# Performance work log

Measured on AMD Instinct MI355X. Metric: run time of the kernel, lower is better.

## Reference

```python
import jax, jax.numpy as jnp
import numpy as np

B, N, M = 256, 4096, 64
EPS = 1e-16

def setup_inputs() -> dict:
    key = jax.random.key(0)
    ks = jax.random.split(key, 9)
    memory = jax.random.normal(ks[0], (B, N, M), dtype=jnp.float32) * 0.1
    k = jax.random.normal(ks[1], (B, M), dtype=jnp.float32)
    beta = jax.random.uniform(ks[2], (B, 1), dtype=jnp.float32) * 5.0  # key strength > 0
    g = jax.random.uniform(ks[3], (B, 1), dtype=jnp.float32)           # gate in [0,1)
    s = jax.nn.softmax(jax.random.normal(ks[4], (B, 3), dtype=jnp.float32), axis=1)  # shift dist
    gamma = 1.0 + jax.random.uniform(ks[5], (B, 1), dtype=jnp.float32) * 2.0  # sharpen >= 1
    w_prev = jax.nn.softmax(jax.random.normal(ks[6], (B, N), dtype=jnp.float32), axis=1)
    e = jax.random.uniform(ks[7], (B, M), dtype=jnp.float32)  # erase in [0,1)
    a = jax.random.normal(ks[8], (B, M), dtype=jnp.float32)   # add vector
    return {"memory": memory, "k": k, "beta": beta, "g": g, "s": s,
            "gamma": gamma, "w_prev": w_prev, "e": e, "a": a}


def reference(memory, k, beta, g, s, gamma, w_prev, e, a):
    # --- address (section 3.3) ---
    # cosine similarity (torch F.cosine_similarity semantics: norms clamped at 1e-8)
    mem_e = memory + EPS                       # [B,N,M]
    k_e = (k + EPS)[:, None, :]                # [B,1,M]
    num = jnp.sum(mem_e * k_e, axis=-1)        # [B,N]
    mem_n = jnp.maximum(jnp.sqrt(jnp.sum(mem_e * mem_e, axis=-1)), 1e-8)
    k_n = jnp.maximum(jnp.sqrt(jnp.sum(k_e * k_e, axis=-1)), 1e-8)
    cos = num / (mem_n * k_n)                  # [B,N]
    wc = jax.nn.softmax(beta * cos, axis=1)    # content weighting
    # interpolate with previous weighting
    wg = g * wc + (1.0 - g) * w_prev           # [B,N]
    # circular convolution with 3-tap shift kernel s:
    # out[n] = s0*wg[n-1] + s1*wg[n] + s2*wg[n+1]  (circular)
    w_hat = (s[:, 0:1] * jnp.roll(wg, 1, axis=1)
             + s[:, 1:2] * wg
             + s[:, 2:3] * jnp.roll(wg, -1, axis=1))
    # sharpen
    wp = w_hat ** gamma
    w = wp / (jnp.sum(wp, axis=1, keepdims=True) + EPS)
    # --- read (section 3.1) ---
    rd = jnp.einsum('bn,bnm->bm', w, memory)
    # --- write (section 3.2): erase then add via outer products ---
    erase = w[:, :, None] * e[:, None, :]      # [B,N,M]
    add = w[:, :, None] * a[:, None, :]        # [B,N,M]
    new_mem = memory * (1.0 - erase) + add
    return rd, new_mem, w
```

## Files before the change

### kernel.cpp

```cpp
#include <hip/hip_runtime.h>
#include <math.h>

#define Bdim 256
#define Ndim 4096
#define Mdim 64
#define EPSF 1e-16f

__global__ __launch_bounds__(256) void pass_a_kernel(
    const float* __restrict__ mem, const float* __restrict__ k,
    float* __restrict__ q)
{
    const int blocks_per_b = Ndim / 64;
    const int b = blockIdx.x / blocks_per_b;
    const int rowbase = (blockIdx.x % blocks_per_b) * 64;
    const int t = threadIdx.x;
    const int m4 = t & 15;
    const int rsub = t >> 4;

    float4 ke = reinterpret_cast<const float4*>(k + b * Mdim)[m4];
    ke.x += EPSF; ke.y += EPSF; ke.z += EPSF; ke.w += EPSF;

    const float4* memb = reinterpret_cast<const float4*>(mem + (size_t)b * Ndim * Mdim);

    #pragma unroll
    for (int it = 0; it < 4; ++it) {
        const int row = rowbase + it * 16 + rsub;
        float4 mv = memb[row * 16 + m4];
        mv.x += EPSF; mv.y += EPSF; mv.z += EPSF; mv.w += EPSF;
        float d  = mv.x * ke.x + mv.y * ke.y + mv.z * ke.z + mv.w * ke.w;
        float nr = mv.x * mv.x + mv.y * mv.y + mv.z * mv.z + mv.w * mv.w;
        #pragma unroll
        for (int mask = 1; mask < 16; mask <<= 1) {
            d  += __shfl_xor(d, mask);
            nr += __shfl_xor(nr, mask);
        }
        if (m4 == 0) {
            const float mn = fmaxf(sqrtf(nr), 1e-8f);
            q[b * Ndim + row] = d / mn;
        }
    }
}

__device__ __forceinline__ float block_reduce_sum(float v, float* red, int t)
{
    const int lane = t & 63, wave = t >> 6;
    #pragma unroll
    for (int mask = 32; mask; mask >>= 1) v += __shfl_xor(v, mask);
    __syncthreads();
    if (lane == 0) red[wave] = v;
    __syncthreads();
    return red[0] + red[1] + red[2] + red[3];
}

__device__ __forceinline__ float block_reduce_max(float v, float* red, int t)
{
    const int lane = t & 63, wave = t >> 6;
    #pragma unroll
    for (int mask = 32; mask; mask >>= 1) v = fmaxf(v, __shfl_xor(v, mask));
    __syncthreads();
    if (lane == 0) red[wave] = v;
    __syncthreads();
    return fmaxf(fmaxf(red[0], red[1]), fmaxf(red[2], red[3]));
}

__global__ __launch_bounds__(256) void pass_b_kernel(
    const float* __restrict__ q, const float* __restrict__ k,
    const float* __restrict__ beta, const float* __restrict__ g,
    const float* __restrict__ s, const float* __restrict__ gamma,
    const float* __restrict__ w_prev, float* __restrict__ w_out)
{
    __shared__ float wg_lds[Ndim];
    __shared__ float red[4];
    __shared__ float sh_kn;

    const int b = blockIdx.x;
    const int t = threadIdx.x;
    const int lane = t & 63, wave = t >> 6;

    if (wave == 0) {
        float v = k[b * Mdim + lane] + EPSF;
        float sq = v * v;
        #pragma unroll
        for (int mask = 32; mask; mask >>= 1) sq += __shfl_xor(sq, mask);
        if (lane == 0) sh_kn = fmaxf(sqrtf(sq), 1e-8f);
    }
    __syncthreads();

    const float beta_eff = beta[b] / sh_kn;
    const float gb = g[b];
    const float s0 = s[b * 3 + 0], s1 = s[b * 3 + 1], s2 = s[b * 3 + 2];
    const float gam = gamma[b];

    const float4* q4  = reinterpret_cast<const float4*>(q + (size_t)b * Ndim);
    const float4* wp4 = reinterpret_cast<const float4*>(w_prev + (size_t)b * Ndim);

    float4 zv[4];
    float zmax = -1e30f;
    #pragma unroll
    for (int i = 0; i < 4; ++i) {
        float4 v = q4[t + i * 256];
        v.x *= beta_eff; v.y *= beta_eff; v.z *= beta_eff; v.w *= beta_eff;
        zv[i] = v;
        zmax = fmaxf(zmax, fmaxf(fmaxf(v.x, v.y), fmaxf(v.z, v.w)));
    }
    zmax = block_reduce_max(zmax, red, t);

    float esum = 0.f;
    #pragma unroll
    for (int i = 0; i < 4; ++i) {
        zv[i].x = expf(zv[i].x - zmax); zv[i].y = expf(zv[i].y - zmax);
        zv[i].z = expf(zv[i].z - zmax); zv[i].w = expf(zv[i].w - zmax);
        esum += zv[i].x + zv[i].y + zv[i].z + zv[i].w;
    }
    esum = block_reduce_sum(esum, red, t);
    const float inv_esum = 1.0f / esum;

    float4 wgv[4];
    #pragma unroll
    for (int i = 0; i < 4; ++i) {
        float4 wp = wp4[t + i * 256];
        float4 w;
        w.x = gb * (zv[i].x * inv_esum) + (1.f - gb) * wp.x;
        w.y = gb * (zv[i].y * inv_esum) + (1.f - gb) * wp.y;
        w.z = gb * (zv[i].z * inv_esum) + (1.f - gb) * wp.z;
        w.w = gb * (zv[i].w * inv_esum) + (1.f - gb) * wp.w;
        wgv[i] = w;
        reinterpret_cast<float4*>(wg_lds)[t + i * 256] = w;
    }
    __syncthreads();

    float4 wpv[4];
    float psum = 0.f;
    #pragma unroll
    for (int i = 0; i < 4; ++i) {
        const int n0 = 4 * (t + i * 256);
        const float left  = wg_lds[(n0 + Ndim - 1) & (Ndim - 1)];
        const float right = wg_lds[(n0 + 4) & (Ndim - 1)];
        const float4 w = wgv[i];
        float4 h;
        h.x = s0 * left + s1 * w.x + s2 * w.y;
        h.y = s0 * w.x  + s1 * w.y + s2 * w.z;
        h.z = s0 * w.y  + s1 * w.z + s2 * w.w;
        h.w = s0 * w.z  + s1 * w.w + s2 * right;
        h.x = powf(h.x, gam); h.y = powf(h.y, gam);
        h.z = powf(h.z, gam); h.w = powf(h.w, gam);
        wpv[i] = h;
        psum += h.x + h.y + h.z + h.w;
    }
    psum = block_reduce_sum(psum, red, t);
    const float inv_psum = 1.0f / (psum + EPSF);

    float4* wout4 = reinterpret_cast<float4*>(w_out + (size_t)b * Ndim);
    #pragma unroll
    for (int i = 0; i < 4; ++i) {
        float4 h = wpv[i];
        h.x *= inv_psum; h.y *= inv_psum; h.z *= inv_psum; h.w *= inv_psum;
        wout4[t + i * 256] = h;
    }
}

#define NCHUNK_C 8

__global__ __launch_bounds__(256) void pass_c_kernel(
    const float* __restrict__ mem, const float* __restrict__ e,
    const float* __restrict__ a, const float* __restrict__ w,
    float* __restrict__ rd, float* __restrict__ new_mem)
{
    const int b = blockIdx.x / NCHUNK_C;
    const int chunk = blockIdx.x % NCHUNK_C;
    const int rowbase = chunk * (Ndim / NCHUNK_C);
    const int t = threadIdx.x;
    const int m4 = t & 15;
    const int rsub = t >> 4;
    const int lane = t & 63, wave = t >> 6;

    float4 ev = reinterpret_cast<const float4*>(e + b * Mdim)[m4];
    float4 av = reinterpret_cast<const float4*>(a + b * Mdim)[m4];

    const float4* memb = reinterpret_cast<const float4*>(mem + (size_t)b * Ndim * Mdim);
    float4* nmb = reinterpret_cast<float4*>(new_mem + (size_t)b * Ndim * Mdim);
    const float* wb = w + (size_t)b * Ndim;

    float4 acc = {0.f, 0.f, 0.f, 0.f};

    #pragma unroll 4
    for (int it = 0; it < (Ndim / NCHUNK_C) / 16; ++it) {
        const int row = rowbase + it * 16 + rsub;
        const float wr = wb[row];
        float4 mv = memb[row * 16 + m4];
        acc.x += wr * mv.x; acc.y += wr * mv.y;
        acc.z += wr * mv.z; acc.w += wr * mv.w;
        float4 nm;
        nm.x = mv.x * (1.f - wr * ev.x) + wr * av.x;
        nm.y = mv.y * (1.f - wr * ev.y) + wr * av.y;
        nm.z = mv.z * (1.f - wr * ev.z) + wr * av.z;
        nm.w = mv.w * (1.f - wr * ev.w) + wr * av.w;
        nmb[row * 16 + m4] = nm;
    }

    #pragma unroll
    for (int mask = 16; mask <= 32; mask <<= 1) {
        acc.x += __shfl_xor(acc.x, mask);
        acc.y += __shfl_xor(acc.y, mask);
        acc.z += __shfl_xor(acc.z, mask);
        acc.w += __shfl_xor(acc.w, mask);
    }

    __shared__ float4 redc[4][16];
    if (lane < 16) redc[wave][lane] = acc;
    __syncthreads();

    if (t < 16) {
        float4 tot = redc[0][t];
        #pragma unroll
        for (int wv = 1; wv < 4; ++wv) {
            tot.x += redc[wv][t].x; tot.y += redc[wv][t].y;
            tot.z += redc[wv][t].z; tot.w += redc[wv][t].w;
        }
        float* dst = rd + b * Mdim + t * 4;
        atomicAdd(dst + 0, tot.x);
        atomicAdd(dst + 1, tot.y);
        atomicAdd(dst + 2, tot.z);
        atomicAdd(dst + 3, tot.w);
    }
}

extern "C" void kernel_launch(void* const* d_in, const int* in_sizes, int n_in,
                              void* d_out, int out_size, void* d_ws, size_t ws_size,
                              hipStream_t stream)
{
    const float* mem    = (const float*)d_in[0];
    const float* k      = (const float*)d_in[1];
    const float* beta   = (const float*)d_in[2];
    const float* g      = (const float*)d_in[3];
    const float* s      = (const float*)d_in[4];
    const float* gamma  = (const float*)d_in[5];
    const float* w_prev = (const float*)d_in[6];
    const float* e      = (const float*)d_in[7];
    const float* a      = (const float*)d_in[8];

    float* out     = (float*)d_out;
    float* rd      = out;
    float* new_mem = out + Bdim * Mdim;
    float* w_out   = out + Bdim * Mdim + (size_t)Bdim * Ndim * Mdim;

    float* q = (float*)d_ws;

    hipMemsetAsync(rd, 0, Bdim * Mdim * sizeof(float), stream);

    pass_a_kernel<<<Bdim * (Ndim / 64), 256, 0, stream>>>(mem, k, q);
    pass_b_kernel<<<Bdim, 256, 0, stream>>>(q, k, beta, g, s, gamma, w_prev, w_out);
    pass_c_kernel<<<Bdim * NCHUNK_C, 256, 0, stream>>>(mem, e, a, w_out, rd, new_mem);
}
```

Before: 520.5 us.

## Reverse pass C traversal for cache reuse, nontemporal stores, fold rd zeroing

Pass C now walks batches and rows in reverse order, so the most recently read memory rows from pass A are likely still in the last-level cache when pass C starts. The new_mem writes use nontemporal stores to avoid evicting those cached rows, and the arithmetic uses native vector types. The separate memset of rd is removed and folded into pass B, which saves one launch. The reversed order depends on cache size and eviction behaviour.

```diff
diff --git a/kernel.cpp b/kernel.cpp
--- a/kernel.cpp
+++ b/kernel.cpp
@@ -5,6 +5,8 @@
 #define Ndim 4096
 #define Mdim 64
 #define EPSF 1e-16f
+
+typedef float vf4 __attribute__((ext_vector_type(4)));
 
 __global__ __launch_bounds__(256) void pass_a_kernel(
     const float* __restrict__ mem, const float* __restrict__ k,
@@ -67,7 +69,8 @@
     const float* __restrict__ q, const float* __restrict__ k,
     const float* __restrict__ beta, const float* __restrict__ g,
     const float* __restrict__ s, const float* __restrict__ gamma,
-    const float* __restrict__ w_prev, float* __restrict__ w_out)
+    const float* __restrict__ w_prev, float* __restrict__ w_out,
+    float* __restrict__ rd)
 {
     __shared__ float wg_lds[Ndim];
     __shared__ float red[4];
@@ -76,6 +79,8 @@
     const int b = blockIdx.x;
     const int t = threadIdx.x;
     const int lane = t & 63, wave = t >> 6;
+
+    if (wave == 1) rd[b * Mdim + lane] = 0.0f;
 
     if (wave == 0) {
         float v = k[b * Mdim + lane] + EPSF;
@@ -166,36 +171,35 @@
     const float* __restrict__ a, const float* __restrict__ w,
     float* __restrict__ rd, float* __restrict__ new_mem)
 {
-    const int b = blockIdx.x / NCHUNK_C;
-    const int chunk = blockIdx.x % NCHUNK_C;
+    const int idx = (Bdim * NCHUNK_C - 1) - (int)blockIdx.x;
+    const int b = idx / NCHUNK_C;
+    const int chunk = idx % NCHUNK_C;
     const int rowbase = chunk * (Ndim / NCHUNK_C);
     const int t = threadIdx.x;
     const int m4 = t & 15;
     const int rsub = t >> 4;
     const int lane = t & 63, wave = t >> 6;
 
-    float4 ev = reinterpret_cast<const float4*>(e + b * Mdim)[m4];
-    float4 av = reinterpret_cast<const float4*>(a + b * Mdim)[m4];
-
-    const float4* memb = reinterpret_cast<const float4*>(mem + (size_t)b * Ndim * Mdim);
-    float4* nmb = reinterpret_cast<float4*>(new_mem + (size_t)b * Ndim * Mdim);
+    float4 ev4 = reinterpret_cast<const float4*>(e + b * Mdim)[m4];
+    float4 av4 = reinterpret_cast<const float4*>(a + b * Mdim)[m4];
+    vf4 ev = {ev4.x, ev4.y, ev4.z, ev4.w};
+    vf4 av = {av4.x, av4.y, av4.z, av4.w};
+
+    const vf4* memb = reinterpret_cast<const vf4*>(mem + (size_t)b * Ndim * Mdim);
+    vf4* nmb = reinterpret_cast<vf4*>(new_mem + (size_t)b * Ndim * Mdim);
     const float* wb = w + (size_t)b * Ndim;
 
-    float4 acc = {0.f, 0.f, 0.f, 0.f};
+    vf4 acc = {0.f, 0.f, 0.f, 0.f};
 
     #pragma unroll 4
-    for (int it = 0; it < (Ndim / NCHUNK_C) / 16; ++it) {
+    for (int it2 = 0; it2 < (Ndim / NCHUNK_C) / 16; ++it2) {
+        const int it = ((Ndim / NCHUNK_C) / 16 - 1) - it2;
         const int row = rowbase + it * 16 + rsub;
         const float wr = wb[row];
-        float4 mv = memb[row * 16 + m4];
-        acc.x += wr * mv.x; acc.y += wr * mv.y;
-        acc.z += wr * mv.z; acc.w += wr * mv.w;
-        float4 nm;
-        nm.x = mv.x * (1.f - wr * ev.x) + wr * av.x;
-        nm.y = mv.y * (1.f - wr * ev.y) + wr * av.y;
-        nm.z = mv.z * (1.f - wr * ev.z) + wr * av.z;
-        nm.w = mv.w * (1.f - wr * ev.w) + wr * av.w;
-        nmb[row * 16 + m4] = nm;
+        vf4 mv = memb[row * 16 + m4];
+        acc += wr * mv;
+        vf4 nm = mv * (1.f - wr * ev) + wr * av;
+        __builtin_nontemporal_store(nm, &nmb[row * 16 + m4]);
     }
 
     #pragma unroll
@@ -206,17 +210,14 @@
         acc.w += __shfl_xor(acc.w, mask);
     }
 
-    __shared__ float4 redc[4][16];
+    __shared__ vf4 redc[4][16];
     if (lane < 16) redc[wave][lane] = acc;
     __syncthreads();
 
     if (t < 16) {
-        float4 tot = redc[0][t];
+        vf4 tot = redc[0][t];
         #pragma unroll
-        for (int wv = 1; wv < 4; ++wv) {
-            tot.x += redc[wv][t].x; tot.y += redc[wv][t].y;
-            tot.z += redc[wv][t].z; tot.w += redc[wv][t].w;
-        }
+        for (int wv = 1; wv < 4; ++wv) tot += redc[wv][t];
         float* dst = rd + b * Mdim + t * 4;
         atomicAdd(dst + 0, tot.x);
         atomicAdd(dst + 1, tot.y);
@@ -246,9 +247,7 @@
 
     float* q = (float*)d_ws;
 
-    hipMemsetAsync(rd, 0, Bdim * Mdim * sizeof(float), stream);
-
     pass_a_kernel<<<Bdim * (Ndim / 64), 256, 0, stream>>>(mem, k, q);
-    pass_b_kernel<<<Bdim, 256, 0, stream>>>(q, k, beta, g, s, gamma, w_prev, w_out);
+    pass_b_kernel<<<Bdim, 256, 0, stream>>>(q, k, beta, g, s, gamma, w_prev, w_out, rd);
     pass_c_kernel<<<Bdim * NCHUNK_C, 256, 0, stream>>>(mem, e, a, w_out, rd, new_mem);
 }
```

New measurement: 505.4 us. 2.9% less time.
